# Kernel tuning notes

Measured on AMD Instinct MI355X. Metric: run time of the kernel, lower is better.

Reference implementation:

```python
import jax, jax.numpy as jnp
import numpy as np
import math

EMBED = 1024
HEADS = 16
HEAD_DIM = EMBED // HEADS


def setup_inputs() -> dict:
    key = jax.random.key(0)
    ks = jax.random.split(key, 6)
    scale = 1.0 / math.sqrt(EMBED)
    x = jax.random.normal(ks[0], (4, 2048, EMBED), dtype=jnp.float32)
    Wv = jax.random.normal(ks[1], (EMBED, EMBED), dtype=jnp.float32) * scale
    Wk = jax.random.normal(ks[2], (EMBED, EMBED), dtype=jnp.float32) * scale
    Wq = jax.random.normal(ks[3], (EMBED, EMBED), dtype=jnp.float32) * scale
    Wo = jax.random.normal(ks[4], (EMBED, EMBED), dtype=jnp.float32) * scale
    bo = jax.random.normal(ks[5], (EMBED,), dtype=jnp.float32) * 0.02
    return {"x": x, "Wq": Wq, "Wk": Wk, "Wv": Wv, "Wo": Wo, "bo": bo}


def reference(x, Wq, Wk, Wv, Wo, bo):
    N, S, E = x.shape
    H, D = HEADS, HEAD_DIM
    # Linear(E,E,bias=False): y = x @ W.T ; weights here stored as [out,in]
    q = (x @ Wq.T).reshape(N, S, H, D)
    k = (x @ Wk.T).reshape(N, S, H, D)
    v = (x @ Wv.T).reshape(N, S, H, D)
    energy = jnp.einsum('nqhd,nkhd->nhqk', q, k)  # [N,H,S,S]
    attn = jax.nn.softmax(energy / math.sqrt(D), axis=-1)
    out = jnp.einsum('nhql,nlhd->nqhd', attn, v).reshape(N, S, E)
    return out @ Wo.T + bo
```

## Files before the change

kernel.cpp:

```cpp
#include <hip/hip_runtime.h>
#include <stdint.h>

#define NB   4
#define SLEN 2048
#define EMB  1024
#define NH   16
#define HD   64
#define MTOT (NB * SLEN)

typedef __bf16 bf8_t  __attribute__((ext_vector_type(8)));
typedef __bf16 bf4_t  __attribute__((ext_vector_type(4)));
typedef float  f4_t   __attribute__((ext_vector_type(4)));

#if __has_builtin(__builtin_amdgcn_exp2f)
#define EXP2(x) __builtin_amdgcn_exp2f(x)
#else
#define EXP2(x) exp2f(x)
#endif

__device__ __forceinline__ void gld16(const void* g, void* l) {
    __builtin_amdgcn_global_load_lds(
        (__attribute__((address_space(1))) void*)(g),
        (__attribute__((address_space(3))) void*)(l),
        16, 0, 0);
}

__device__ __forceinline__ uint32_t pack_bf16_rtn(float a, float b) {
    uint32_t ua = __builtin_bit_cast(uint32_t, a) + 0x8000u;
    uint32_t ub = __builtin_bit_cast(uint32_t, b) + 0x8000u;
    return __builtin_amdgcn_perm(ub, ua, 0x07060302u);
}
__device__ __forceinline__ uint32_t pack_bf16_rtz(float a, float b) {
    return __builtin_amdgcn_perm(__builtin_bit_cast(uint32_t, b),
                                 __builtin_bit_cast(uint32_t, a), 0x07060302u);
}

__global__ __launch_bounds__(256) void cast_all(const float* __restrict__ x,
                                                const float* __restrict__ Wq,
                                                const float* __restrict__ Wk,
                                                const float* __restrict__ Wv,
                                                const float* __restrict__ Wo,
                                                __bf16* __restrict__ xb,
                                                __bf16* __restrict__ wb) {
    int b = blockIdx.x;
    const float* s;
    __bf16* d;
    if (b < 8192) {
        s = x; d = xb;
    } else {
        int y = (b - 8192) >> 10;
        s = (y == 0) ? Wq : (y == 1) ? Wk : (y == 2) ? Wv : Wo;
        d = wb + (size_t)y * (EMB * EMB);
        b = (b - 8192) & 1023;
    }
    int i = (b * 256 + (int)threadIdx.x) * 4;
    float4 f = *(const float4*)(s + i);
    bf4_t o = { (__bf16)f.x, (__bf16)f.y, (__bf16)f.z, (__bf16)f.w };
    *(bf4_t*)(d + i) = o;
}

__device__ __forceinline__ void gstage(const __bf16* __restrict__ A,
                                       const __bf16* __restrict__ B,
                                       int m0, int n0, int k0, int K, int tid,
                                       __bf16* __restrict__ As,
                                       __bf16* __restrict__ Bs) {
#pragma unroll
    for (int t = 0; t < 4; ++t) {
        int c   = t * 256 + tid;
        int row = c >> 3;
        int kc  = (c & 7) ^ (row & 7);
        int cb  = c & ~63;
        gld16(A + (size_t)(m0 + row) * K + k0 + kc * 8, As + cb * 8);
        gld16(B + (size_t)(n0 + row) * K + k0 + kc * 8, Bs + cb * 8);
    }
}

template <bool SWAP>
__device__ __forceinline__ void gcompute(const __bf16* __restrict__ As,
                                         const __bf16* __restrict__ Bs,
                                         f4_t (*acc)[4],
                                         int wm, int wn, int quad, int l16) {
#pragma unroll
    for (int ks = 0; ks < 2; ++ks) {
        bf8_t af[4], bfr[4];
#pragma unroll
        for (int i = 0; i < 4; ++i) {
            int r = wm + i * 16 + l16;
            af[i] = *(const bf8_t*)&As[r * 64 + (((ks * 4 + quad) ^ (r & 7)) * 8)];
        }
#pragma unroll
        for (int j = 0; j < 4; ++j) {
            int r = wn + j * 16 + l16;
            bfr[j] = *(const bf8_t*)&Bs[r * 64 + (((ks * 4 + quad) ^ (r & 7)) * 8)];
        }
#pragma unroll
        for (int i = 0; i < 4; ++i)
#pragma unroll
            for (int j = 0; j < 4; ++j) {
                if (SWAP)
                    acc[i][j] = __builtin_amdgcn_mfma_f32_16x16x32_bf16(
                        bfr[j], af[i], acc[i][j], 0, 0, 0);
                else
                    acc[i][j] = __builtin_amdgcn_mfma_f32_16x16x32_bf16(
                        af[i], bfr[j], acc[i][j], 0, 0, 0);
            }
    }
}

template <bool SWAP>
__device__ __forceinline__ void gkloop(const __bf16* __restrict__ A,
                                       const __bf16* __restrict__ B,
                                       int m0, int n0, int K, int tid,
                                       __bf16* As0, __bf16* Bs0,
                                       __bf16* As1, __bf16* Bs1,
                                       f4_t (*acc)[4],
                                       int wm, int wn, int quad, int l16) {
    gstage(A, B, m0, n0, 0, K, tid, As0, Bs0);
    for (int k0 = 0; k0 < K; k0 += 128) {
        __syncthreads();
        gstage(A, B, m0, n0, k0 + 64, K, tid, As1, Bs1);
        gcompute<SWAP>(As0, Bs0, acc, wm, wn, quad, l16);
        __syncthreads();
        int knn = (k0 + 128 < K) ? k0 + 128 : k0 + 64;
        gstage(A, B, m0, n0, knn, K, tid, As0, Bs0);
        gcompute<SWAP>(As1, Bs1, acc, wm, wn, quad, l16);
    }
}

__global__ __launch_bounds__(256, 2) void proj_qkv(const __bf16* __restrict__ A,
                                                   const __bf16* __restrict__ B,
                                                   __bf16* __restrict__ qb) {
    __shared__ __bf16 As0[128 * 64], Bs0[128 * 64];
    __shared__ __bf16 As1[128 * 64], Bs1[128 * 64];

    const int tid  = threadIdx.x;
    const int lane = tid & 63;
    const int w    = tid >> 6;
    const int quad = lane >> 4;
    const int l16  = lane & 15;
    const int m0   = blockIdx.x * 128;
    const int n0   = blockIdx.y * 128;
    const int wm   = (w >> 1) * 64;
    const int wn   = (w & 1) * 64;

    f4_t acc[4][4];
#pragma unroll
    for (int i = 0; i < 4; ++i)
#pragma unroll
        for (int j = 0; j < 4; ++j) acc[i][j] = (f4_t){0.f, 0.f, 0.f, 0.f};

    if (n0 < 2048) {
        gkloop<true>(A, B, m0, n0, EMB, tid, As0, Bs0, As1, Bs1, acc, wm, wn, quad, l16);
#pragma unroll
        for (int i = 0; i < 4; ++i)
#pragma unroll
            for (int j = 0; j < 4; ++j) {
                int m   = m0 + wm + i * 16 + l16;
                int col = n0 + wn + j * 16 + quad * 4;
                __bf16* dst = (col < 1024) ? qb : qb + (size_t)8 * 1024 * 1024;
                bf4_t pk = { (__bf16)acc[i][j][0], (__bf16)acc[i][j][1],
                             (__bf16)acc[i][j][2], (__bf16)acc[i][j][3] };
                *(bf4_t*)&dst[(size_t)m * 1024 + (col & 1023)] = pk;
            }
    } else {
        gkloop<false>(A, B, m0, n0, EMB, tid, As0, Bs0, As1, Bs1, acc, wm, wn, quad, l16);
        __bf16* vtb = qb + (size_t)16 * 1024 * 1024;
#pragma unroll
        for (int i = 0; i < 4; ++i)
#pragma unroll
            for (int j = 0; j < 4; ++j) {
                int m  = m0 + wm + i * 16 + quad * 4;
                int ch = n0 - 2048 + wn + j * 16 + l16;
                size_t idx = ((size_t)(m >> 11) * 1024 + ch) * 2048 + (m & 2047);
                bf4_t pk = { (__bf16)acc[i][j][0], (__bf16)acc[i][j][1],
                             (__bf16)acc[i][j][2], (__bf16)acc[i][j][3] };
                *(bf4_t*)&vtb[idx] = pk;
            }
    }
}

__global__ __launch_bounds__(256, 2) void gemm_out(const __bf16* __restrict__ A,
                                                   const __bf16* __restrict__ B,
                                                   float* __restrict__ C,
                                                   const float* __restrict__ bias) {
    __shared__ __bf16 As0[128 * 64], Bs0[128 * 64];
    __shared__ __bf16 As1[128 * 64], Bs1[128 * 64];

    const int tid  = threadIdx.x;
    const int lane = tid & 63;
    const int w    = tid >> 6;
    const int quad = lane >> 4;
    const int l16  = lane & 15;
    const int m0   = blockIdx.x * 128;
    const int n0   = blockIdx.y * 128;
    const int wm   = (w >> 1) * 64;
    const int wn   = (w & 1) * 64;

    f4_t acc[4][4];
#pragma unroll
    for (int i = 0; i < 4; ++i)
#pragma unroll
        for (int j = 0; j < 4; ++j) acc[i][j] = (f4_t){0.f, 0.f, 0.f, 0.f};

    gkloop<true>(A, B, m0, n0, EMB, tid, As0, Bs0, As1, Bs1, acc, wm, wn, quad, l16);

#pragma unroll
    for (int i = 0; i < 4; ++i)
#pragma unroll
        for (int j = 0; j < 4; ++j) {
            int m   = m0 + wm + i * 16 + l16;
            int col = n0 + wn + j * 16 + quad * 4;
            float4 bv = *(const float4*)&bias[col];
            float4 ov = { acc[i][j][0] + bv.x, acc[i][j][1] + bv.y,
                          acc[i][j][2] + bv.z, acc[i][j][3] + bv.w };
            *(float4*)&C[(size_t)m * EMB + col] = ov;
        }
}

__device__ __forceinline__ void attn_stage(const __bf16* __restrict__ kbase,
                                           const __bf16* __restrict__ vbase,
                                           int l0, int tid,
                                           __bf16* __restrict__ Ksb,
                                           __bf16* __restrict__ Vsb) {
#pragma unroll
    for (int t = 0; t < 2; ++t) {
        int c   = t * 256 + tid;
        int row = c >> 3;
        int kc  = (c & 7) ^ (row & 7);
        int cb  = c & ~63;
        gld16(kbase + (size_t)(l0 + row) * EMB + kc * 8, Ksb + cb * 8);
        gld16(vbase + (size_t)row * SLEN + l0 + kc * 8, Vsb + cb * 8);
    }
}

__device__ __forceinline__ void attn_tile(const __bf16* __restrict__ Ksb,
                                          const __bf16* __restrict__ Vsb,
                                          __bf16* __restrict__ pw,
                                          const bf8_t (*bq)[2], bf8_t aones,
                                          f4_t* ls, f4_t (*o)[4],
                                          int quad, int l16, int sw) {
#pragma unroll
    for (int jk = 0; jk < 4; ++jk) {
        bf8_t ak[2];
#pragma unroll
        for (int ks = 0; ks < 2; ++ks)
            ak[ks] = *(const bf8_t*)&Ksb[(jk * 16 + l16) * 64 +
                                         (((ks * 4 + quad) ^ sw) * 8)];
#pragma unroll
        for (int jq = 0; jq < 4; ++jq) {
            f4_t e = (f4_t){0.f, 0.f, 0.f, 0.f};
            e = __builtin_amdgcn_mfma_f32_16x16x32_bf16(ak[0], bq[jq][0], e, 0, 0, 0);
            e = __builtin_amdgcn_mfma_f32_16x16x32_bf16(ak[1], bq[jq][1], e, 0, 0, 0);
            uint32_t d0 = pack_bf16_rtz(EXP2(e[0]), EXP2(e[1]));
            uint32_t d1 = pack_bf16_rtz(EXP2(e[2]), EXP2(e[3]));
            *(uint2*)&pw[(jq * 16 + l16) * 72 + jk * 16 + quad * 4] = (uint2){d0, d1};
        }
    }
#pragma unroll
    for (int ks = 0; ks < 2; ++ks) {
        bf8_t bp[4];
#pragma unroll
        for (int jq = 0; jq < 4; ++jq)
            bp[jq] = *(const bf8_t*)&pw[(jq * 16 + l16) * 72 + ks * 32 + quad * 8];
#pragma unroll
        for (int jq = 0; jq < 4; ++jq)
            ls[jq] = __builtin_amdgcn_mfma_f32_16x16x32_bf16(aones, bp[jq], ls[jq], 0, 0, 0);
#pragma unroll
        for (int jd = 0; jd < 4; ++jd) {
            bf8_t av = *(const bf8_t*)&Vsb[(jd * 16 + l16) * 64 +
                                           (((ks * 4 + quad) ^ sw) * 8)];
#pragma unroll
            for (int jq = 0; jq < 4; ++jq)
                o[jq][jd] = __builtin_amdgcn_mfma_f32_16x16x32_bf16(av, bp[jq],
                                                                    o[jq][jd], 0, 0, 0);
        }
    }
}

__global__ __launch_bounds__(256, 2) void attn_fwd(const __bf16* __restrict__ Q,
                                                   const __bf16* __restrict__ K,
                                                   const __bf16* __restrict__ Vt,
                                                   __bf16* __restrict__ O) {
    __shared__ __bf16 Ks0[64 * 64];
    __shared__ __bf16 Ks1[64 * 64];
    __shared__ __bf16 Vs0[64 * 64];
    __shared__ __bf16 Vs1[64 * 64];
    __shared__ __bf16 Ps[4 * 64 * 72];

    const int tid  = threadIdx.x;
    const int lane = tid & 63;
    const int w    = tid >> 6;
    const int quad = lane >> 4;
    const int l16  = lane & 15;
    const int nh   = blockIdx.y;
    const int n    = nh >> 4;
    const int h    = nh & 15;
    const int q0   = blockIdx.x * 256 + w * 64;

    const float QSCALE = 0.125f * 1.44269504f;

    bf8_t bq[4][2];
#pragma unroll
    for (int jq = 0; jq < 4; ++jq)
#pragma unroll
        for (int ks = 0; ks < 2; ++ks) {
            bf8_t v = *(const bf8_t*)(Q + (size_t)(n * SLEN + q0 + jq * 16 + l16) * EMB +
                                      h * HD + ks * 32 + quad * 8);
#pragma unroll
            for (int t = 0; t < 8; ++t) v[t] = (__bf16)((float)v[t] * QSCALE);
            bq[jq][ks] = v;
        }

    bf8_t aones;
#pragma unroll
    for (int t = 0; t < 8; ++t) aones[t] = (__bf16)1.0f;

    f4_t ls[4];
    f4_t o[4][4];
#pragma unroll
    for (int jq = 0; jq < 4; ++jq) {
        ls[jq] = (f4_t){0.f, 0.f, 0.f, 0.f};
#pragma unroll
        for (int jd = 0; jd < 4; ++jd) o[jq][jd] = (f4_t){0.f, 0.f, 0.f, 0.f};
    }

    const __bf16* kbase = K + (size_t)n * SLEN * EMB + h * HD;
    const __bf16* vbase = Vt + (size_t)nh * HD * SLEN;
    __bf16* pw = Ps + w * 64 * 72;
    const int sw = l16 & 7;

    attn_stage(kbase, vbase, 0, tid, Ks0, Vs0);

    for (int it = 0; it < 32; it += 2) {
        int l0 = it * 64;
        __syncthreads();
        attn_stage(kbase, vbase, l0 + 64, tid, Ks1, Vs1);
        attn_tile(Ks0, Vs0, pw, bq, aones, ls, o, quad, l16, sw);
        __syncthreads();
        int lnn = (l0 + 128 < SLEN) ? l0 + 128 : l0 + 64;
        attn_stage(kbase, vbase, lnn, tid, Ks0, Vs0);
        attn_tile(Ks1, Vs1, pw, bq, aones, ls, o, quad, l16, sw);
    }

#pragma unroll
    for (int jq = 0; jq < 4; ++jq) {
        float inv = 1.0f / ls[jq][0];
#pragma unroll
        for (int jd = 0; jd < 4; ++jd) {
            uint32_t d0 = pack_bf16_rtn(o[jq][jd][0] * inv, o[jq][jd][1] * inv);
            uint32_t d1 = pack_bf16_rtn(o[jq][jd][2] * inv, o[jq][jd][3] * inv);
            *(uint2*)&O[(size_t)(n * SLEN + q0 + jq * 16 + l16) * EMB + h * HD +
                        jd * 16 + quad * 4] = (uint2){d0, d1};
        }
    }
}

extern "C" void kernel_launch(void* const* d_in, const int* in_sizes, int n_in,
                              void* d_out, int out_size, void* d_ws, size_t ws_size,
                              hipStream_t stream) {
    const float* x  = (const float*)d_in[0];
    const float* Wq = (const float*)d_in[1];
    const float* Wk = (const float*)d_in[2];
    const float* Wv = (const float*)d_in[3];
    const float* Wo = (const float*)d_in[4];
    const float* bo = (const float*)d_in[5];

    char* wsb = (char*)d_ws;
    const size_t MB = (size_t)1 << 20;
    __bf16* xb  = (__bf16*)(wsb + 0 * MB);
    __bf16* ab  = xb;
    __bf16* wqb = (__bf16*)(wsb + 16 * MB);
    __bf16* wob = (__bf16*)(wsb + 22 * MB);
    __bf16* qb  = (__bf16*)(wsb + 24 * MB);
    __bf16* kb  = (__bf16*)(wsb + 40 * MB);
    __bf16* vtb = (__bf16*)(wsb + 56 * MB);

    cast_all<<<dim3(12288), dim3(256), 0, stream>>>(x, Wq, Wk, Wv, Wo, xb, wqb);

    proj_qkv<<<dim3(MTOT / 128, 3072 / 128), 256, 0, stream>>>(xb, wqb, qb);

    attn_fwd<<<dim3(SLEN / 256, NB * NH), 256, 0, stream>>>(qb, kb, vtb, ab);

    gemm_out<<<dim3(MTOT / 128, EMB / 128), 256, 0, stream>>>(ab, wob, (float*)d_out, bo);
}
```

Before: 262.3 us.

## Keep attention probabilities in registers via permlane swaps instead of LDS round-trip

The exponentiated scores are now packed into registers and rearranged into the B-operand layout for the PV and row-sum MFMAs using permlane32/permlane16 swap instructions, rather than being written to and read back from a per-wave LDS scratch buffer. The loop is restructured so each half of the key tile is computed and consumed immediately. Removing the Ps buffer shrinks shared memory, and launch bounds are raised to 3 blocks per SM to exploit the higher occupancy. The higher occupancy target may force register pressure or spills.

```diff
diff --git a/kernel.cpp b/kernel.cpp
--- a/kernel.cpp
+++ b/kernel.cpp
@@ -11,6 +11,8 @@
 typedef __bf16 bf8_t  __attribute__((ext_vector_type(8)));
 typedef __bf16 bf4_t  __attribute__((ext_vector_type(4)));
 typedef float  f4_t   __attribute__((ext_vector_type(4)));
+typedef unsigned int u32x2 __attribute__((ext_vector_type(2)));
+typedef unsigned int u32x4 __attribute__((ext_vector_type(4)));
 
 #if __has_builtin(__builtin_amdgcn_exp2f)
 #define EXP2(x) __builtin_amdgcn_exp2f(x)
@@ -235,33 +237,35 @@
 
 __device__ __forceinline__ void attn_tile(const __bf16* __restrict__ Ksb,
                                           const __bf16* __restrict__ Vsb,
-                                          __bf16* __restrict__ pw,
                                           const bf8_t (*bq)[2], bf8_t aones,
                                           f4_t* ls, f4_t (*o)[4],
                                           int quad, int l16, int sw) {
 #pragma unroll
-    for (int jk = 0; jk < 4; ++jk) {
-        bf8_t ak[2];
-#pragma unroll
-        for (int ks = 0; ks < 2; ++ks)
-            ak[ks] = *(const bf8_t*)&Ksb[(jk * 16 + l16) * 64 +
-                                         (((ks * 4 + quad) ^ sw) * 8)];
+    for (int ks = 0; ks < 2; ++ks) {
+        uint32_t pk[4][4];
+#pragma unroll
+        for (int jkl = 0; jkl < 2; ++jkl) {
+            const int jk = ks * 2 + jkl;
+            bf8_t ak0 = *(const bf8_t*)&Ksb[(jk * 16 + l16) * 64 + ((quad ^ sw) * 8)];
+            bf8_t ak1 = *(const bf8_t*)&Ksb[(jk * 16 + l16) * 64 + (((4 + quad) ^ sw) * 8)];
+#pragma unroll
+            for (int jq = 0; jq < 4; ++jq) {
+                f4_t e = (f4_t){0.f, 0.f, 0.f, 0.f};
+                e = __builtin_amdgcn_mfma_f32_16x16x32_bf16(ak0, bq[jq][0], e, 0, 0, 0);
+                e = __builtin_amdgcn_mfma_f32_16x16x32_bf16(ak1, bq[jq][1], e, 0, 0, 0);
+                pk[jq][jkl * 2 + 0] = pack_bf16_rtz(EXP2(e[0]), EXP2(e[1]));
+                pk[jq][jkl * 2 + 1] = pack_bf16_rtz(EXP2(e[2]), EXP2(e[3]));
+            }
+        }
+        bf8_t bp[4];
 #pragma unroll
         for (int jq = 0; jq < 4; ++jq) {
-            f4_t e = (f4_t){0.f, 0.f, 0.f, 0.f};
-            e = __builtin_amdgcn_mfma_f32_16x16x32_bf16(ak[0], bq[jq][0], e, 0, 0, 0);
-            e = __builtin_amdgcn_mfma_f32_16x16x32_bf16(ak[1], bq[jq][1], e, 0, 0, 0);
-            uint32_t d0 = pack_bf16_rtz(EXP2(e[0]), EXP2(e[1]));
-            uint32_t d1 = pack_bf16_rtz(EXP2(e[2]), EXP2(e[3]));
-            *(uint2*)&pw[(jq * 16 + l16) * 72 + jk * 16 + quad * 4] = (uint2){d0, d1};
-        }
-    }
-#pragma unroll
-    for (int ks = 0; ks < 2; ++ks) {
-        bf8_t bp[4];
-#pragma unroll
-        for (int jq = 0; jq < 4; ++jq)
-            bp[jq] = *(const bf8_t*)&pw[(jq * 16 + l16) * 72 + ks * 32 + quad * 8];
+            u32x2 s0 = __builtin_amdgcn_permlane32_swap(pk[jq][0], pk[jq][2], false, false);
+            u32x2 s1 = __builtin_amdgcn_permlane32_swap(pk[jq][1], pk[jq][3], false, false);
+            u32x2 t0 = __builtin_amdgcn_permlane16_swap(s0[0], s0[1], false, false);
+            u32x2 t1 = __builtin_amdgcn_permlane16_swap(s1[0], s1[1], false, false);
+            bp[jq] = __builtin_bit_cast(bf8_t, (u32x4){t0[0], t1[0], t0[1], t1[1]});
+        }
 #pragma unroll
         for (int jq = 0; jq < 4; ++jq)
             ls[jq] = __builtin_amdgcn_mfma_f32_16x16x32_bf16(aones, bp[jq], ls[jq], 0, 0, 0);
@@ -277,7 +281,7 @@
     }
 }
 
-__global__ __launch_bounds__(256, 2) void attn_fwd(const __bf16* __restrict__ Q,
+__global__ __launch_bounds__(256, 3) void attn_fwd(const __bf16* __restrict__ Q,
                                                    const __bf16* __restrict__ K,
                                                    const __bf16* __restrict__ Vt,
                                                    __bf16* __restrict__ O) {
@@ -285,7 +289,6 @@
     __shared__ __bf16 Ks1[64 * 64];
     __shared__ __bf16 Vs0[64 * 64];
     __shared__ __bf16 Vs1[64 * 64];
-    __shared__ __bf16 Ps[4 * 64 * 72];
 
     const int tid  = threadIdx.x;
     const int lane = tid & 63;
@@ -326,7 +329,6 @@
 
     const __bf16* kbase = K + (size_t)n * SLEN * EMB + h * HD;
     const __bf16* vbase = Vt + (size_t)nh * HD * SLEN;
-    __bf16* pw = Ps + w * 64 * 72;
     const int sw = l16 & 7;
 
     attn_stage(kbase, vbase, 0, tid, Ks0, Vs0);
@@ -335,11 +337,11 @@
         int l0 = it * 64;
         __syncthreads();
         attn_stage(kbase, vbase, l0 + 64, tid, Ks1, Vs1);
-        attn_tile(Ks0, Vs0, pw, bq, aones, ls, o, quad, l16, sw);
+        attn_tile(Ks0, Vs0, bq, aones, ls, o, quad, l16, sw);
         __syncthreads();
         int lnn = (l0 + 128 < SLEN) ? l0 + 128 : l0 + 64;
         attn_stage(kbase, vbase, lnn, tid, Ks0, Vs0);
-        attn_tile(Ks1, Vs1, pw, bq, aones, ls, o, quad, l16, sw);
+        attn_tile(Ks1, Vs1, bq, aones, ls, o, quad, l16, sw);
     }
 
 #pragma unroll
```

Result: slower. 333.4 us (+27.1%).
